# Kernel optimization log

Measured on AMD Instinct MI355X. Metric: run time of the kernel, lower is better.

## Reference

```python
import jax, jax.numpy as jnp
import numpy as np

H = 1024
I = 4096
E = 8
B, S, K = 2, 2048, 2


def setup_inputs() -> dict:
    key = jax.random.key(0)
    k1, k2, k3, k4, k5, k6 = jax.random.split(key, 6)
    x = jax.random.normal(k1, (B, S, H), dtype=jnp.float32)
    expert_indices = jax.random.randint(k2, (B, S, K), 0, E, dtype=jnp.int32)
    expert_weights = jax.random.uniform(k3, (B, S, K), dtype=jnp.float32)
    gate_proj = jax.random.normal(k4, (E, I, H), dtype=jnp.float32) * 0.02
    up_proj = jax.random.normal(k5, (E, I, H), dtype=jnp.float32) * 0.02
    down_proj = jax.random.normal(k6, (E, H, I), dtype=jnp.float32) * 0.02
    return {"x": x, "expert_indices": expert_indices, "expert_weights": expert_weights,
            "gate_proj": gate_proj, "up_proj": up_proj, "down_proj": down_proj}


def reference(x, expert_indices, expert_weights, gate_proj, up_proj, down_proj):
    b, s, h = x.shape
    e = gate_proj.shape[0]
    k = expert_indices.shape[-1]
    xf = x.reshape(-1, h)                       # [N, H]
    idx = expert_indices.reshape(-1, k)         # [N, K]
    wts = expert_weights.reshape(-1, k)         # [N, K]
    # combine[n, e] = sum over slots k with idx[n,k]==e of wts[n,k]
    onehot = jax.nn.one_hot(idx, e, dtype=x.dtype)            # [N, K, E]
    combine = jnp.einsum('nk,nke->ne', wts, onehot)           # [N, E]
    out = jnp.zeros_like(xf)
    # Fixed small unrolled loop over experts (data dims fully vectorized).
    for ei in range(e):
        gate = jax.nn.silu(xf @ gate_proj[ei].T)              # [N, I]
        up = xf @ up_proj[ei].T                               # [N, I]
        out = out + ((gate * up) @ down_proj[ei].T) * combine[:, ei:ei + 1]
    return out.reshape(b, s, h)
```

## Files before the change

### kernel.cpp

```cpp
#include <hip/hip_runtime.h>
#include <hip/hip_bf16.h>
#include <cstdint>

#define HD 1024
#define ID 4096
#define NE 8
#define NTOK 4096
#define NASS 8192
#define NWL 72

typedef unsigned short u16;
typedef __attribute__((ext_vector_type(8))) __bf16 bf16x8;
typedef __attribute__((ext_vector_type(4))) float f32x4;

__device__ __forceinline__ void async16(void* lds, const void* g) {
  __builtin_amdgcn_global_load_lds(
      (const __attribute__((address_space(1))) uint32_t*)g,
      (__attribute__((address_space(3))) uint32_t*)lds, 16, 0, 0);
}

__device__ __forceinline__ u16 f2b(float f) {
  __bf16 h = (__bf16)f;
  return __builtin_bit_cast(u16, h);
}

__device__ __forceinline__ bf16x8 cvt8(const float* p) {
  const float4* q = (const float4*)p;
  float4 a = q[0], b = q[1];
  bf16x8 v;
  v[0] = (__bf16)a.x; v[1] = (__bf16)a.y; v[2] = (__bf16)a.z; v[3] = (__bf16)a.w;
  v[4] = (__bf16)b.x; v[5] = (__bf16)b.y; v[6] = (__bf16)b.z; v[7] = (__bf16)b.w;
  return v;
}

__global__ void k_pre(const float* __restrict__ x, const float* __restrict__ gate,
                      const float* __restrict__ up, u16* __restrict__ xb,
                      u16* __restrict__ wg, u16* __restrict__ wu) {
  int bid = blockIdx.x, t = threadIdx.x;
  const float* src; u16* dst; size_t base;
  if (bid < 2048)        { src = x;    dst = xb; base = (size_t)bid * 256; }
  else if (bid < 18432)  { src = gate; dst = wg; base = (size_t)(bid - 2048) * 256; }
  else                   { src = up;   dst = wu; base = (size_t)(bid - 18432) * 256; }
  size_t i8 = (base + t) * 8;
  *(bf16x8*)(dst + i8) = cvt8(src + i8);
}

__global__ void k_meta(const int* __restrict__ eidx, int* __restrict__ offsets,
                       int* __restrict__ wl, int* __restrict__ tokl) {
  __shared__ int cnt[NE], offs_s[NE + 1], cur[NE];
  int t = threadIdx.x;
  if (t < NE) cnt[t] = 0;
  __syncthreads();
  for (int i = t; i < NASS; i += 1024) atomicAdd(&cnt[eidx[i]], 1);
  __syncthreads();
  if (t == 0) {
    int s = 0;
    for (int e = 0; e < NE; ++e) { offs_s[e] = s; s += cnt[e]; }
    offs_s[NE] = s;
    int w = 0;
    for (int e = 0; e < NE; ++e)
      for (int mt = 0; mt * 128 < cnt[e]; ++mt) wl[w++] = (e << 16) | mt;
    for (; w < NWL; ++w) wl[w] = -1;
  }
  if (t < NE) cur[t] = 0;
  __syncthreads();
  for (int i = t; i < NASS; i += 1024) {
    int e = eidx[i];
    int p = atomicAdd(&cur[e], 1);
    tokl[offs_s[e] + p] = i;
  }
  if (t <= NE) offsets[t] = offs_s[t];
}

__global__ __launch_bounds__(256, 2) void k_g1(
    const u16* __restrict__ xb, const u16* __restrict__ wg, const u16* __restrict__ wu,
    const float* __restrict__ down, u16* __restrict__ wd,
    const int* __restrict__ offsets, const int* __restrict__ wl,
    const int* __restrict__ tokl, u16* __restrict__ interm) {
  const int bx = blockIdx.x;
  const int t = threadIdx.x;
  if (bx >= 32) {
    int cid = (bx - 32) + 32 * (int)blockIdx.y;
    if (cid < 2048) {
#pragma unroll
      for (int l = 0; l < 8; ++l) {
        size_t i8 = (((size_t)cid * 8 + l) * 256 + t) * 8;
        *(bf16x8*)(wd + i8) = cvt8(down + i8);
      }
    }
    return;
  }
  const int wle = wl[blockIdx.y];
  if (wle < 0) return;
  const int e = wle >> 16;
  const int m0 = (wle & 0xffff) << 7;
  const int offs = offsets[e];
  const int Me = offsets[e + 1] - offs;
  const int n0 = bx * 128;
  const int lane = t & 63, wv = t >> 6;
  const int wm = wv & 1, wn = wv >> 1;

  __shared__ __align__(16) u16 As[128 * 64];
  __shared__ __align__(16) u16 Bg[128 * 64];
  __shared__ __align__(16) u16 Bu[128 * 64];

  const u16* asrc[4];
#pragma unroll
  for (int p = 0; p < 4; ++p) {
    int c = p * 256 + t;
    int r = c >> 3, c8 = c & 7;
    int row = m0 + r; if (row > Me - 1) row = Me - 1;
    asrc[p] = xb + (size_t)(tokl[offs + row] >> 1) * HD + c8 * 8;
  }
  const u16 *bgsrc[4], *busrc[4];
#pragma unroll
  for (int p = 0; p < 4; ++p) {
    int c = p * 256 + t;
    int r = c >> 3, c8 = c & 7;
    size_t boff = ((size_t)e * ID + n0 + r) * HD + c8 * 8;
    bgsrc[p] = wg + boff;
    busrc[p] = wu + boff;
  }

  f32x4 accg[4][4], accu[4][4];
#pragma unroll
  for (int mi = 0; mi < 4; ++mi)
#pragma unroll
    for (int ni = 0; ni < 4; ++ni) {
      accg[mi][ni] = (f32x4){0.f, 0.f, 0.f, 0.f};
      accu[mi][ni] = (f32x4){0.f, 0.f, 0.f, 0.f};
    }

  const int lrow = lane & 15, lk = (lane >> 4) * 8;
#pragma unroll 1
  for (int ks = 0; ks < HD / 64; ++ks) {
    __syncthreads();
#pragma unroll
    for (int p = 0; p < 4; ++p) {
      async16((char*)As + (p * 256 + wv * 64) * 16, asrc[p]);
      async16((char*)Bg + (p * 256 + wv * 64) * 16, bgsrc[p]);
      async16((char*)Bu + (p * 256 + wv * 64) * 16, busrc[p]);
    }
    __syncthreads();
#pragma unroll
    for (int kk = 0; kk < 2; ++kk) {
      bf16x8 af[4], bg[4], bu[4];
#pragma unroll
      for (int mi = 0; mi < 4; ++mi)
        af[mi] = *(const bf16x8*)&As[(wm * 64 + mi * 16 + lrow) * 64 + kk * 32 + lk];
#pragma unroll
      for (int ni = 0; ni < 4; ++ni) {
        bg[ni] = *(const bf16x8*)&Bg[(wn * 64 + ni * 16 + lrow) * 64 + kk * 32 + lk];
        bu[ni] = *(const bf16x8*)&Bu[(wn * 64 + ni * 16 + lrow) * 64 + kk * 32 + lk];
      }
#pragma unroll
      for (int mi = 0; mi < 4; ++mi)
#pragma unroll
        for (int ni = 0; ni < 4; ++ni) {
          accg[mi][ni] = __builtin_amdgcn_mfma_f32_16x16x32_bf16(af[mi], bg[ni], accg[mi][ni], 0, 0, 0);
          accu[mi][ni] = __builtin_amdgcn_mfma_f32_16x16x32_bf16(af[mi], bu[ni], accu[mi][ni], 0, 0, 0);
        }
    }
#pragma unroll
    for (int p = 0; p < 4; ++p) { asrc[p] += 64; bgsrc[p] += 64; busrc[p] += 64; }
  }

#pragma unroll
  for (int mi = 0; mi < 4; ++mi) {
    int rb = wm * 64 + mi * 16 + (lane >> 4) * 4;
#pragma unroll
    for (int ni = 0; ni < 4; ++ni) {
      int col = n0 + wn * 64 + ni * 16 + (lane & 15);
#pragma unroll
      for (int j = 0; j < 4; ++j) {
        int row = m0 + rb + j;
        if (row < Me) {
          float g = accg[mi][ni][j], u = accu[mi][ni][j];
          float s = g / (1.f + __expf(-g));
          interm[(size_t)(offs + row) * ID + col] = f2b(s * u);
        }
      }
    }
  }
}

__global__ __launch_bounds__(256) void k_g2(
    const u16* __restrict__ interm, const u16* __restrict__ wd,
    const int* __restrict__ offsets, const int* __restrict__ wl,
    const int* __restrict__ tokl, float* __restrict__ buf) {
  const int wle = wl[blockIdx.y];
  if (wle < 0) return;
  const int e = wle >> 16;
  const int m0 = (wle & 0xffff) << 7;
  const int offs = offsets[e];
  const int Me = offsets[e + 1] - offs;
  const int n0 = blockIdx.x * 128;
  const int t = threadIdx.x, lane = t & 63, wv = t >> 6;
  const int wm = wv & 1, wn = wv >> 1;

  __shared__ __align__(16) u16 As[128 * 64];
  __shared__ __align__(16) u16 Bs[128 * 64];

  const u16* asrc[4];
#pragma unroll
  for (int p = 0; p < 4; ++p) {
    int c = p * 256 + t;
    int r = c >> 3, c8 = c & 7;
    int row = m0 + r; if (row > Me - 1) row = Me - 1;
    asrc[p] = interm + (size_t)(offs + row) * ID + c8 * 8;
  }
  const u16* bsrc[4];
#pragma unroll
  for (int p = 0; p < 4; ++p) {
    int c = p * 256 + t;
    int r = c >> 3, c8 = c & 7;
    bsrc[p] = wd + ((size_t)e * HD + n0 + r) * ID + c8 * 8;
  }

  f32x4 acc[4][4];
#pragma unroll
  for (int mi = 0; mi < 4; ++mi)
#pragma unroll
    for (int ni = 0; ni < 4; ++ni) acc[mi][ni] = (f32x4){0.f, 0.f, 0.f, 0.f};

  const int lrow = lane & 15, lk = (lane >> 4) * 8;
#pragma unroll 1
  for (int ks = 0; ks < ID / 64; ++ks) {
    __syncthreads();
#pragma unroll
    for (int p = 0; p < 4; ++p) {
      async16((char*)As + (p * 256 + wv * 64) * 16, asrc[p]);
      async16((char*)Bs + (p * 256 + wv * 64) * 16, bsrc[p]);
    }
    __syncthreads();
#pragma unroll
    for (int kk = 0; kk < 2; ++kk) {
      bf16x8 af[4], bfr[4];
#pragma unroll
      for (int mi = 0; mi < 4; ++mi)
        af[mi] = *(const bf16x8*)&As[(wm * 64 + mi * 16 + lrow) * 64 + kk * 32 + lk];
#pragma unroll
      for (int ni = 0; ni < 4; ++ni)
        bfr[ni] = *(const bf16x8*)&Bs[(wn * 64 + ni * 16 + lrow) * 64 + kk * 32 + lk];
#pragma unroll
      for (int mi = 0; mi < 4; ++mi)
#pragma unroll
        for (int ni = 0; ni < 4; ++ni)
          acc[mi][ni] = __builtin_amdgcn_mfma_f32_16x16x32_bf16(af[mi], bfr[ni], acc[mi][ni], 0, 0, 0);
    }
#pragma unroll
    for (int p = 0; p < 4; ++p) { asrc[p] += 64; bsrc[p] += 64; }
  }

#pragma unroll
  for (int mi = 0; mi < 4; ++mi) {
    int rb = wm * 64 + mi * 16 + (lane >> 4) * 4;
#pragma unroll
    for (int j = 0; j < 4; ++j) {
      int row = m0 + rb + j;
      if (row < Me) {
        int aid = tokl[offs + row];
#pragma unroll
        for (int ni = 0; ni < 4; ++ni) {
          int col = n0 + wn * 64 + ni * 16 + (lane & 15);
          buf[(size_t)aid * HD + col] = acc[mi][ni][j];
        }
      }
    }
  }
}

__global__ void k_final(const float* __restrict__ buf, const float* __restrict__ ewt,
                        float* __restrict__ out) {
  size_t idx = (size_t)blockIdx.x * 256 + threadIdx.x;
  int tok = (int)(idx >> 8);
  int c4 = (int)(idx & 255);
  const float4* b0 = (const float4*)(buf + (size_t)(2 * tok) * HD) + c4;
  const float4* b1 = (const float4*)(buf + (size_t)(2 * tok + 1) * HD) + c4;
  float w0 = ewt[2 * tok], w1 = ewt[2 * tok + 1];
  float4 a = *b0, b = *b1;
  float4 r = {w0 * a.x + w1 * b.x, w0 * a.y + w1 * b.y,
              w0 * a.z + w1 * b.z, w0 * a.w + w1 * b.w};
  ((float4*)(out + (size_t)tok * HD))[c4] = r;
}

extern "C" void kernel_launch(void* const* d_in, const int* in_sizes, int n_in,
                              void* d_out, int out_size, void* d_ws, size_t ws_size,
                              hipStream_t stream) {
  const float* x    = (const float*)d_in[0];
  const int*   eidx = (const int*)d_in[1];
  const float* ewt  = (const float*)d_in[2];
  const float* gate = (const float*)d_in[3];
  const float* up   = (const float*)d_in[4];
  const float* down = (const float*)d_in[5];
  float* out = (float*)d_out;
  char* ws = (char*)d_ws;

  constexpr size_t OFF_INTERM = 0;
  constexpr size_t OFF_XB     = 67108864;
  constexpr size_t OFF_META   = 75497472;
  constexpr size_t OFF_TOK    = 75498496;
  constexpr size_t OFF_WD     = 75531264;
  constexpr size_t OFF_WG     = 142640128;
  constexpr size_t OFF_WU     = 209748992;

  u16* interm  = (u16*)(ws + OFF_INTERM);
  u16* xb      = (u16*)(ws + OFF_XB);
  int* offsets = (int*)(ws + OFF_META);
  int* wl      = (int*)(ws + OFF_META + 64);
  int* tokl    = (int*)(ws + OFF_TOK);
  u16* wd      = (u16*)(ws + OFF_WD);
  u16* wg      = (u16*)(ws + OFF_WG);
  u16* wu      = (u16*)(ws + OFF_WU);
  float* buf   = (float*)(ws + OFF_WG);

  k_pre<<<dim3(34816), dim3(256), 0, stream>>>(x, gate, up, xb, wg, wu);
  k_meta<<<dim3(1), dim3(1024), 0, stream>>>(eidx, offsets, wl, tokl);
  k_g1<<<dim3(64, NWL), dim3(256), 0, stream>>>(xb, wg, wu, down, wd, offsets, wl, tokl, interm);
  k_g2<<<dim3(HD / 128, NWL), dim3(256), 0, stream>>>(interm, wd, offsets, wl, tokl, buf);
  k_final<<<dim3(4096), dim3(256), 0, stream>>>(buf, ewt, out);
}
```

Before: 483.9 us.

## Fuse weighted combine into down-proj GEMM via atomics, widen its N tile

The separate k_final combine kernel and its fp32 scratch buffer are removed. The down-projection kernel now scales each row by its routing weight and atomically adds it into the output, which k_pre zeroes alongside the x conversion. The down GEMM tile widens from 128 to 256 output columns, halving the number of blocks and the reloads of the interm tiles. Launch bounds are raised for both GEMMs. The catch is fp32 atomic traffic and contention on the output, higher register pressure from 32 accumulators per thread, and fewer blocks for k_g2.

New measurement: 633.7 us. 1.31x slower.

```diff
diff --git a/kernel.cpp b/kernel.cpp
--- a/kernel.cpp
+++ b/kernel.cpp
@@ -35,12 +35,20 @@
 
 __global__ void k_pre(const float* __restrict__ x, const float* __restrict__ gate,
                       const float* __restrict__ up, u16* __restrict__ xb,
-                      u16* __restrict__ wg, u16* __restrict__ wu) {
+                      u16* __restrict__ wg, u16* __restrict__ wu,
+                      float* __restrict__ out) {
   int bid = blockIdx.x, t = threadIdx.x;
+  if (bid < 2048) {
+    size_t i8 = ((size_t)bid * 256 + t) * 8;
+    *(bf16x8*)(xb + i8) = cvt8(x + i8);
+    float4 z = {0.f, 0.f, 0.f, 0.f};
+    float4* op = (float4*)(out + i8);
+    op[0] = z; op[1] = z;
+    return;
+  }
   const float* src; u16* dst; size_t base;
-  if (bid < 2048)        { src = x;    dst = xb; base = (size_t)bid * 256; }
-  else if (bid < 18432)  { src = gate; dst = wg; base = (size_t)(bid - 2048) * 256; }
-  else                   { src = up;   dst = wu; base = (size_t)(bid - 18432) * 256; }
+  if (bid < 18432) { src = gate; dst = wg; base = (size_t)(bid - 2048) * 256; }
+  else             { src = up;   dst = wu; base = (size_t)(bid - 18432) * 256; }
   size_t i8 = (base + t) * 8;
   *(bf16x8*)(dst + i8) = cvt8(src + i8);
 }
@@ -72,7 +80,7 @@
   if (t <= NE) offsets[t] = offs_s[t];
 }
 
-__global__ __launch_bounds__(256, 2) void k_g1(
+__global__ __launch_bounds__(256, 3) void k_g1(
     const u16* __restrict__ xb, const u16* __restrict__ wg, const u16* __restrict__ wu,
     const float* __restrict__ down, u16* __restrict__ wd,
     const int* __restrict__ offsets, const int* __restrict__ wl,
@@ -184,22 +192,23 @@
   }
 }
 
-__global__ __launch_bounds__(256) void k_g2(
+__global__ __launch_bounds__(256, 2) void k_g2(
     const u16* __restrict__ interm, const u16* __restrict__ wd,
     const int* __restrict__ offsets, const int* __restrict__ wl,
-    const int* __restrict__ tokl, float* __restrict__ buf) {
+    const int* __restrict__ tokl, const float* __restrict__ ewt,
+    float* __restrict__ out) {
   const int wle = wl[blockIdx.y];
   if (wle < 0) return;
   const int e = wle >> 16;
   const int m0 = (wle & 0xffff) << 7;
   const int offs = offsets[e];
   const int Me = offsets[e + 1] - offs;
-  const int n0 = blockIdx.x * 128;
+  const int n0 = blockIdx.x * 256;
   const int t = threadIdx.x, lane = t & 63, wv = t >> 6;
   const int wm = wv & 1, wn = wv >> 1;
 
   __shared__ __align__(16) u16 As[128 * 64];
-  __shared__ __align__(16) u16 Bs[128 * 64];
+  __shared__ __align__(16) u16 Bs[256 * 64];
 
   const u16* asrc[4];
 #pragma unroll
@@ -209,47 +218,50 @@
     int row = m0 + r; if (row > Me - 1) row = Me - 1;
     asrc[p] = interm + (size_t)(offs + row) * ID + c8 * 8;
   }
-  const u16* bsrc[4];
-#pragma unroll
-  for (int p = 0; p < 4; ++p) {
+  const u16* bsrc[8];
+#pragma unroll
+  for (int p = 0; p < 8; ++p) {
     int c = p * 256 + t;
     int r = c >> 3, c8 = c & 7;
     bsrc[p] = wd + ((size_t)e * HD + n0 + r) * ID + c8 * 8;
   }
 
-  f32x4 acc[4][4];
+  f32x4 acc[4][8];
 #pragma unroll
   for (int mi = 0; mi < 4; ++mi)
 #pragma unroll
-    for (int ni = 0; ni < 4; ++ni) acc[mi][ni] = (f32x4){0.f, 0.f, 0.f, 0.f};
+    for (int ni = 0; ni < 8; ++ni) acc[mi][ni] = (f32x4){0.f, 0.f, 0.f, 0.f};
 
   const int lrow = lane & 15, lk = (lane >> 4) * 8;
 #pragma unroll 1
   for (int ks = 0; ks < ID / 64; ++ks) {
     __syncthreads();
 #pragma unroll
-    for (int p = 0; p < 4; ++p) {
+    for (int p = 0; p < 4; ++p)
       async16((char*)As + (p * 256 + wv * 64) * 16, asrc[p]);
+#pragma unroll
+    for (int p = 0; p < 8; ++p)
       async16((char*)Bs + (p * 256 + wv * 64) * 16, bsrc[p]);
-    }
     __syncthreads();
 #pragma unroll
     for (int kk = 0; kk < 2; ++kk) {
-      bf16x8 af[4], bfr[4];
+      bf16x8 af[4], bfr[8];
 #pragma unroll
       for (int mi = 0; mi < 4; ++mi)
         af[mi] = *(const bf16x8*)&As[(wm * 64 + mi * 16 + lrow) * 64 + kk * 32 + lk];
 #pragma unroll
-      for (int ni = 0; ni < 4; ++ni)
-        bfr[ni] = *(const bf16x8*)&Bs[(wn * 64 + ni * 16 + lrow) * 64 + kk * 32 + lk];
+      for (int ni = 0; ni < 8; ++ni)
+        bfr[ni] = *(const bf16x8*)&Bs[(wn * 128 + ni * 16 + lrow) * 64 + kk * 32 + lk];
 #pragma unroll
       for (int mi = 0; mi < 4; ++mi)
 #pragma unroll
-        for (int ni = 0; ni < 4; ++ni)
+        for (int ni = 0; ni < 8; ++ni)
           acc[mi][ni] = __builtin_amdgcn_mfma_f32_16x16x32_bf16(af[mi], bfr[ni], acc[mi][ni], 0, 0, 0);
     }
 #pragma unroll
-    for (int p = 0; p < 4; ++p) { asrc[p] += 64; bsrc[p] += 64; }
+    for (int p = 0; p < 4; ++p) asrc[p] += 64;
+#pragma unroll
+    for (int p = 0; p < 8; ++p) bsrc[p] += 64;
   }
 
 #pragma unroll
@@ -260,28 +272,16 @@
       int row = m0 + rb + j;
       if (row < Me) {
         int aid = tokl[offs + row];
-#pragma unroll
-        for (int ni = 0; ni < 4; ++ni) {
-          int col = n0 + wn * 64 + ni * 16 + (lane & 15);
-          buf[(size_t)aid * HD + col] = acc[mi][ni][j];
+        float w = ewt[aid];
+        float* orow = out + (size_t)(aid >> 1) * HD;
+#pragma unroll
+        for (int ni = 0; ni < 8; ++ni) {
+          int col = n0 + wn * 128 + ni * 16 + (lane & 15);
+          atomicAdd(orow + col, w * acc[mi][ni][j]);
         }
       }
     }
   }
-}
-
-__global__ void k_final(const float* __restrict__ buf, const float* __restrict__ ewt,
-                        float* __restrict__ out) {
-  size_t idx = (size_t)blockIdx.x * 256 + threadIdx.x;
-  int tok = (int)(idx >> 8);
-  int c4 = (int)(idx & 255);
-  const float4* b0 = (const float4*)(buf + (size_t)(2 * tok) * HD) + c4;
-  const float4* b1 = (const float4*)(buf + (size_t)(2 * tok + 1) * HD) + c4;
-  float w0 = ewt[2 * tok], w1 = ewt[2 * tok + 1];
-  float4 a = *b0, b = *b1;
-  float4 r = {w0 * a.x + w1 * b.x, w0 * a.y + w1 * b.y,
-              w0 * a.z + w1 * b.z, w0 * a.w + w1 * b.w};
-  ((float4*)(out + (size_t)tok * HD))[c4] = r;
 }
 
 extern "C" void kernel_launch(void* const* d_in, const int* in_sizes, int n_in,
@@ -312,11 +312,9 @@
   u16* wd      = (u16*)(ws + OFF_WD);
   u16* wg      = (u16*)(ws + OFF_WG);
   u16* wu      = (u16*)(ws + OFF_WU);
-  float* buf   = (float*)(ws + OFF_WG);
-
-  k_pre<<<dim3(34816), dim3(256), 0, stream>>>(x, gate, up, xb, wg, wu);
+
+  k_pre<<<dim3(34816), dim3(256), 0, stream>>>(x, gate, up, xb, wg, wu, out);
   k_meta<<<dim3(1), dim3(1024), 0, stream>>>(eidx, offsets, wl, tokl);
   k_g1<<<dim3(64, NWL), dim3(256), 0, stream>>>(xb, wg, wu, down, wd, offsets, wl, tokl, interm);
-  k_g2<<<dim3(HD / 128, NWL), dim3(256), 0, stream>>>(interm, wd, offsets, wl, tokl, buf);
-  k_final<<<dim3(4096), dim3(256), 0, stream>>>(buf, ewt, out);
-}
+  k_g2<<<dim3(HD / 256, NWL), dim3(256), 0, stream>>>(interm, wd, offsets, wl, tokl, ewt, out);
+}
```
